# Kernel tuning notes

Measured on AMD Instinct MI355X. Metric: run time of the kernel, lower is better.

Reference implementation:

```python
import jax, jax.numpy as jnp
import numpy as np

# NSA hyperparams (match init_kwargs)
KS, ST, SEL, TOPN, WIN = 32, 16, 64, 16, 512
NEG = -1e30  # additive mask value (finite so fp32 softmax stays stable)


def setup_inputs() -> dict:
    key = jax.random.key(0)
    ks = jax.random.split(key, 6)
    B, S, Hq, Hk, D, Dv = 1, 2048, 16, 2, 128, 128
    q = jax.random.normal(ks[0], (B, S, Hq, D), jnp.float32)
    k = jax.random.normal(ks[1], (B, S, Hk, D), jnp.float32)
    v = jax.random.normal(ks[2], (B, S, Hk, Dv), jnp.float32)
    # learned per-position compression weights for K and V blocks
    w_cmp_k = jax.random.normal(ks[3], (KS,), jnp.float32) / KS
    w_cmp_v = jax.random.normal(ks[4], (KS,), jnp.float32) / KS
    # gating head: Linear(qk_head_dim, 3) -> sigmoid
    w_gate = jax.random.normal(ks[5], (D, 3), jnp.float32) * 0.02
    b_gate = jnp.zeros((3,), jnp.float32)
    return dict(q=q, k=k, v=v, w_cmp_k=w_cmp_k, w_cmp_v=w_cmp_v,
                w_gate=w_gate, b_gate=b_gate)


def _nsa(q, k, v, w_cmp_k, w_cmp_v, w_gate, b_gate):
    B, S, Hq, D = q.shape
    Hk = k.shape[2]
    G = Hq // Hk                      # GQA group size
    Dv = v.shape[-1]
    scale = D ** -0.5
    t_pos = jnp.arange(S)

    # ---- 1. compressed-KV attention (CompressAttn) ----
    T = (S - KS) // ST + 1            # number of compressed blocks
    widx = jnp.arange(T)[:, None] * ST + jnp.arange(KS)[None, :]   # [T, KS]
    cmp_k = jnp.einsum('btknd,k->btnd', k[:, widx], w_cmp_k)        # [B,T,Hk,D]
    cmp_v = jnp.einsum('btknd,k->btnd', v[:, widx], w_cmp_v)        # [B,T,Hk,Dv]

    qg = q.reshape(B, S, Hk, G, D)
    s_cmp = jnp.einsum('bsngd,btnd->bngst', qg, cmp_k) * scale      # [B,Hk,G,S,T]
    blk_end = jnp.arange(T) * ST + KS - 1
    cmp_mask = blk_end[None, :] <= t_pos[:, None]                   # [S,T] block fully past
    p_cmp = jax.nn.softmax(jnp.where(cmp_mask, s_cmp, NEG), axis=-1)
    p_cmp = p_cmp * cmp_mask          # zero rows with no visible block
    cmp_o = jnp.einsum('bngst,btnd->bsngd', p_cmp, cmp_v).reshape(B, S, Hq, Dv)

    # ---- 2. top-n selection-block scoring (select_for_fwd_bwd) ----
    NSel = S // SEL
    starts = jnp.arange(T) * ST
    b_lo = starts // SEL
    b_hi = (starts + KS - 1) // SEL
    bidx = jnp.arange(NSel)
    # map compressed-block probs onto overlapping selection blocks
    Mmap = ((bidx[None, :] >= b_lo[:, None]) & (bidx[None, :] <= b_hi[:, None])).astype(q.dtype)  # [T,NSel]
    p_slc = jnp.einsum('bngst,tm->bnsm', p_cmp, Mmap)               # sum over group g -> [B,Hk,S,NSel]

    cur_blk = t_pos // SEL
    blk_causal = (bidx[None, :] * SEL) <= t_pos[:, None]            # [S,NSel]
    forced = (bidx[None, :] == 0) | (bidx[None, :] == cur_blk[:, None])
    blk_score = jnp.where(forced, -NEG, p_slc)                      # always keep block 0 + current
    blk_score = jnp.where(blk_causal, blk_score, NEG)
    vals, inds = jax.lax.top_k(blk_score, TOPN)                     # [B,Hk,S,TOPN]
    valid = (vals > NEG / 2).astype(q.dtype)
    sel_blk_mask = (jax.nn.one_hot(inds, NSel, dtype=q.dtype) * valid[..., None]).sum(-2) > 0  # [B,Hk,S,NSel]

    # ---- 3. block-sparse selected attention (select_attn) ----
    tok_sel_mask = jnp.repeat(sel_blk_mask, SEL, axis=-1)           # [B,Hk,S,S]
    causal = t_pos[None, :] <= t_pos[:, None]                       # [S,S]
    tok_sel_mask = tok_sel_mask & causal
    s_tok = jnp.einsum('bsngd,bjnd->bngsj', qg, k) * scale          # [B,Hk,G,S,S] shared scores
    p_sel = jax.nn.softmax(jnp.where(tok_sel_mask[:, :, None], s_tok, NEG), axis=-1)
    sel_o = jnp.einsum('bngsj,bjnd->bsngd', p_sel, v).reshape(B, S, Hq, Dv)

    win_mask = causal & ((t_pos[:, None] - t_pos[None, :]) <= WIN)
    p_win = jax.nn.softmax(jnp.where(win_mask, s_tok, NEG), axis=-1)
    win_o = jnp.einsum('bngsj,bjnd->bsngd', p_win, v).reshape(B, S, Hq, Dv)

    # ---- 5. learned sigmoid gating combine ----
    gate = jax.nn.sigmoid(jnp.einsum('bshd,dc->bshc', q, w_gate) + b_gate)  # [B,S,Hq,3]
    return (cmp_o * gate[..., 0:1] + sel_o * gate[..., 1:2] + win_o * gate[..., 2:3])


def reference(q, k, v, w_cmp_k, w_cmp_v, w_gate, b_gate):
    return _nsa(q, k, v, w_cmp_k, w_cmp_v, w_gate, b_gate)
```

## Files before the change

### kernel.cpp

```cpp
#include <hip/hip_runtime.h>

#define SS   2048
#define HQ   16
#define HK   2
#define GQ   8
#define DD   128
#define DV   128
#define KS   32
#define ST   16
#define SELB 64
#define TOPN 16
#define WINW 512
#define TT   127
#define NSEL 32
#define QSC  0.12751744f

typedef __attribute__((ext_vector_type(8))) short bf16x8;
typedef __attribute__((ext_vector_type(4))) float f32x4;

#if defined(__has_builtin)
#  if __has_builtin(__builtin_amdgcn_exp2f)
#    define EXP2(x) __builtin_amdgcn_exp2f(x)
#  endif
#endif
#ifndef EXP2
#  define EXP2(x) __expf((x) * 0.6931471805599453f)
#endif

__device__ __forceinline__ short f2bf(float x) {
    union { float f; unsigned u; } a; a.f = x;
    unsigned r = a.u + 0x7FFFu + ((a.u >> 16) & 1u);
    return (short)(r >> 16);
}
__device__ __forceinline__ float bf2f(short b) {
    union { unsigned u; float f; } x; x.u = ((unsigned)(unsigned short)b) << 16; return x.f;
}

__global__ __launch_bounds__(256) void k_prep(
    const float* __restrict__ k, const float* __restrict__ v,
    const float* __restrict__ wck, const float* __restrict__ wcv,
    const float* __restrict__ wg,
    short* __restrict__ kfr, short* __restrict__ vfr,
    short* __restrict__ ckh, short* __restrict__ ckl,
    short* __restrict__ cvfr, short* __restrict__ wgh, short* __restrict__ wgl)
{
    __shared__ float red[256];
    int bid = blockIdx.x, tid = threadIdx.x;
    int lane = tid & 63, quad = (lane >> 4) & 3, l16 = lane & 15;
    if (bid < 256) {
        int tb = bid >> 1, n = bid & 1;
        int kb = tid >> 6;
        int token = tb * 16 + l16;
        int feat = kb * 32 + quad * 8;
        const float* src = &k[(token * HK + n) * DD + feat];
        bf16x8 t;
        #pragma unroll
        for (int e = 0; e < 8; ++e) t[e] = f2bf(src[e]);
        *(bf16x8*)&kfr[(((n * 128 + tb) * 4 + kb) * 64 + lane) * 8] = t;
    } else if (bid < 512) {
        int id = bid - 256;
        int cb = id >> 3, n = (id >> 2) & 1, it = id & 3;
        int frag = it * 4 + (tid >> 6);
        int h = frag >> 3, f = frag & 7;
        int d = f * 16 + l16;
        int tok0 = cb * 64 + h * 32 + quad * 8;
        bf16x8 t;
        #pragma unroll
        for (int e = 0; e < 8; ++e) t[e] = f2bf(v[((tok0 + e) * HK + n) * DV + d]);
        *(bf16x8*)&vfr[((((n * 32 + cb) * 2 + h) * 8 + f) * 64 + lane) * 8] = t;
    } else if (bid < 768) {
        int id = bid - 512;
        int n = id & 1, t = id >> 1;
        int d = tid & 127, jh = tid >> 7;
        float a = 0.f;
        if (t < TT) {
            #pragma unroll
            for (int jj = 0; jj < 16; ++jj) {
                int j = jh * 16 + jj;
                a += k[((t * ST + j) * HK + n) * DD + d] * wck[j];
            }
        }
        red[tid] = a;
        __syncthreads();
        if (tid < 128) {
            float s = red[tid] + red[tid + 128];
            short hi = f2bf(s);
            short lo = f2bf(s - bf2f(hi));
            int tile = t >> 4, l16i = t & 15;
            int kb = d >> 5, qd = (d >> 3) & 3, e = d & 7;
            int off = (((n * 8 + tile) * 4 + kb) * 64 + qd * 16 + l16i) * 8 + e;
            ckh[off] = hi;
            ckl[off] = lo;
        }
    } else if (bid < 1024) {
        int id = bid - 768;
        int n = id & 1, tok = id >> 1;
        int d = tid & 127, jh = tid >> 7;
        float a = 0.f;
        if (tok < TT) {
            #pragma unroll
            for (int jj = 0; jj < 16; ++jj) {
                int j = jh * 16 + jj;
                a += v[((tok * ST + j) * HK + n) * DV + d] * wcv[j];
            }
        }
        red[tid] = a;
        __syncthreads();
        if (tid < 128) {
            float s = red[tid] + red[tid + 128];
            int w2 = d >> 5, half = (d >> 4) & 1, l16i = d & 15;
            int kb = tok >> 5, qd = (tok >> 3) & 3, e = tok & 7;
            cvfr[((((n * 4 + w2) * 2 + half) * 4 + kb) * 64 + qd * 16 + l16i) * 8 + e] = f2bf(s);
        }
    } else {
        int kb = tid >> 6;
        bf16x8 th, tl;
        #pragma unroll
        for (int e = 0; e < 8; ++e) {
            int kidx = kb * 32 + quad * 8 + e;
            float x = (l16 < 3) ? wg[kidx * 3 + l16] : 0.f;
            th[e] = f2bf(x);
            tl[e] = f2bf(x - bf2f(th[e]));
        }
        *(bf16x8*)&wgh[(kb * 64 + lane) * 8] = th;
        *(bf16x8*)&wgl[(kb * 64 + lane) * 8] = tl;
    }
}

__global__ __launch_bounds__(256, 4) void k_fused(
    const float* __restrict__ q,
    const short* __restrict__ ckh, const short* __restrict__ ckl,
    const short* __restrict__ cvfr,
    const short* __restrict__ kfr, const short* __restrict__ vfr,
    const short* __restrict__ wgh, const short* __restrict__ wgl,
    const float* __restrict__ bg,
    float* __restrict__ out)
{
    int r = (int)blockIdx.x & 7, j = (int)blockIdx.x >> 3;
    int sidx = (j < 64) ? (1023 - r * 64 - j) : (r * 64 + (j - 64));
    int s0 = sidx * 2;
    int s1 = s0 + 1;
    int n = blockIdx.y;
    int tid = threadIdx.x;
    int w = tid >> 6, lane = tid & 63, quad = lane >> 4, l16 = lane & 15;

    __shared__ union {
        float p[16][132];
        short Pw[4][16][64];
        float o2[2][16][68];
    } u;
    __shared__ short OselB[16][128];
    __shared__ short cmpO[16][136];
    __shared__ float g3v[16][3];
    __shared__ float pslc2[2][NSEL];
    __shared__ float lw[4][16];
    __shared__ unsigned selMask[2];
    __shared__ unsigned ublk[NSEL];
    __shared__ int shUCnt;

    f32x4 z4 = {0.f, 0.f, 0.f, 0.f};
    const bf16x8 ones8 = {0x3F80, 0x3F80, 0x3F80, 0x3F80, 0x3F80, 0x3F80, 0x3F80, 0x3F80};

    bf16x8 qb[4];
    bf16x8 qlb[4];
    {
        const float* qpg = &q[((s0 + (l16 >> 3)) * HQ + n * GQ + (l16 & 7)) * DD + quad * 8];
        #pragma unroll
        for (int kb = 0; kb < 4; ++kb) {
            f32x4 x = *(const f32x4*)(qpg + kb * 32);
            f32x4 y = *(const f32x4*)(qpg + kb * 32 + 4);
            bf16x8 th, tl;
            #pragma unroll
            for (int j2 = 0; j2 < 4; ++j2) {
                float xs = x[j2] * QSC, ys = y[j2] * QSC;
                th[j2] = f2bf(xs);     tl[j2] = f2bf(xs - bf2f(th[j2]));
                th[4+j2] = f2bf(ys);   tl[4+j2] = f2bf(ys - bf2f(th[4+j2]));
            }
            qb[kb] = th; qlb[kb] = tl;
        }
    }
    if (w == 0) {
        f32x4 gacc = z4;
        #pragma unroll
        for (int kb = 0; kb < 4; ++kb) {
            bf16x8 wh = *(const bf16x8*)&wgh[(kb * 64 + lane) * 8];
            bf16x8 wl = *(const bf16x8*)&wgl[(kb * 64 + lane) * 8];
            gacc = __builtin_amdgcn_mfma_f32_16x16x32_bf16(wh, qb[kb], gacc, 0, 0, 0);
            gacc = __builtin_amdgcn_mfma_f32_16x16x32_bf16(wl, qb[kb], gacc, 0, 0, 0);
            gacc = __builtin_amdgcn_mfma_f32_16x16x32_bf16(wh, qlb[kb], gacc, 0, 0, 0);
        }
        if (quad == 0) {
            #pragma unroll
            for (int r2 = 0; r2 < 3; ++r2) {
                float a = gacc[r2] * (1.f / QSC) + bg[r2];
                g3v[l16][r2] = 1.f / (1.f + __expf(-a));
            }
        }
    }
    for (int tile = w; tile < 8; tile += 4) {
        const short* khp = &ckh[((n * 8 + tile) * 256 + lane) * 8];
        const short* klp = &ckl[((n * 8 + tile) * 256 + lane) * 8];
        f32x4 acc = z4;
        #pragma unroll
        for (int kb = 0; kb < 4; ++kb) {
            bf16x8 ah = *(const bf16x8*)(khp + kb * 512);
            bf16x8 al = *(const bf16x8*)(klp + kb * 512);
            acc = __builtin_amdgcn_mfma_f32_16x16x32_bf16(ah, qb[kb], acc, 0, 0, 0);
            acc = __builtin_amdgcn_mfma_f32_16x16x32_bf16(al, qb[kb], acc, 0, 0, 0);
            acc = __builtin_amdgcn_mfma_f32_16x16x32_bf16(ah, qlb[kb], acc, 0, 0, 0);
        }
        *(f32x4*)&u.p[l16][tile * 16 + quad * 4] = acc;
    }
    __syncthreads();

    int ntt0 = (s0 >= KS - 1) ? min((s0 - (KS - 1)) / ST + 1, TT) : 0;
    int ntt1 = (s1 >= KS - 1) ? min((s1 - (KS - 1)) / ST + 1, TT) : 0;

    #pragma unroll
    for (int rr = 0; rr < 4; ++rr) {
        int row = w * 4 + rr;
        int ntt = (row < 8) ? ntt0 : ntt1;
        int t1 = lane, t2 = lane + 64;
        float v1 = (t1 < ntt) ? u.p[row][t1] : -1e30f;
        float v2 = (t2 < ntt) ? u.p[row][t2] : -1e30f;
        float m = fmaxf(v1, v2);
        #pragma unroll
        for (int o = 32; o > 0; o >>= 1) m = fmaxf(m, __shfl_xor(m, o, 64));
        float e1 = (t1 < ntt) ? EXP2(v1 - m) : 0.f;
        float e2 = (t2 < ntt) ? EXP2(v2 - m) : 0.f;
        float ssum = e1 + e2;
        #pragma unroll
        for (int o = 32; o > 0; o >>= 1) ssum += __shfl_xor(ssum, o, 64);
        float inv = (ntt > 0) ? (1.f / ssum) : 0.f;
        e1 *= inv; e2 *= inv;
        u.p[row][t1] = e1; u.p[row][t2] = e2;
    }
    __syncthreads();

    if (tid < 64) {
        int p01 = tid >> 5, m = tid & 31;
        float a = 0.f;
        for (int dt = -1; dt < 4; ++dt) {
            int t = 4 * m + dt;
            if (t < 0 || t >= TT) continue;
            bool maps = (t / 4 == m) || ((t % 4 == 3) && (t / 4 == m - 1));
            if (!maps) continue;
            for (int g = 0; g < GQ; ++g) a += u.p[p01 * 8 + g][t];
        }
        pslc2[p01][m] = a;
    }
    __syncthreads();

    if (w < 2) {
        int p01 = w;
        int sp = p01 ? s1 : s0;
        int cur = sp / SELB;
        float v;
        if (lane < NSEL) {
            int m = lane;
            if (m == 0 || m == cur) v = 1e30f;
            else if (m * SELB <= sp) v = pslc2[p01][m];
            else v = -1e30f;
        } else v = -1e31f;
        unsigned msk = 0;
        #pragma unroll
        for (int pick = 0; pick < TOPN; ++pick) {
            float bv = v;
            #pragma unroll
            for (int o = 32; o > 0; o >>= 1) bv = fmaxf(bv, __shfl_xor(bv, o, 64));
            unsigned long long b = __ballot(v == bv);
            int best = __ffsll((long long)b) - 1;
            if (bv > -5e29f) msk |= 1u << best;
            if (lane == best) v = -1e31f;
        }
        if (lane == 0) selMask[p01] = msk;
    }
    {
        f32x4 o0 = z4, o1 = z4;
        int d0 = w * 32 + l16;
        const short* cvp = &cvfr[((n * 4 + w) * 512 + lane) * 8];
        const float* prow = &u.p[l16][quad * 8];
        #pragma unroll
        for (int kb = 0; kb < 4; ++kb) {
            f32x4 x = *(const f32x4*)(prow + kb * 32);
            f32x4 y = *(const f32x4*)(prow + kb * 32 + 4);
            bf16x8 pa;
            #pragma unroll
            for (int j2 = 0; j2 < 4; ++j2) { pa[j2] = f2bf(x[j2]); pa[4+j2] = f2bf(y[j2]); }
            bf16x8 vb0 = *(const bf16x8*)(cvp + kb * 512);
            bf16x8 vb1 = *(const bf16x8*)(cvp + 2048 + kb * 512);
            o0 = __builtin_amdgcn_mfma_f32_16x16x32_bf16(pa, vb0, o0, 0, 0, 0);
            o1 = __builtin_amdgcn_mfma_f32_16x16x32_bf16(pa, vb1, o1, 0, 0, 0);
        }
        #pragma unroll
        for (int r2 = 0; r2 < 4; ++r2) {
            int h2 = quad * 4 + r2;
            cmpO[h2][d0]      = f2bf(o0[r2]);
            cmpO[h2][d0 + 16] = f2bf(o1[r2]);
        }
    }
    __syncthreads();

    if (tid == 0) {
        unsigned m0 = selMask[0], m1 = selMask[1], mu = m0 | m1;
        int uc = 0;
        for (int b = 0; b < NSEL; ++b)
            if ((mu >> b) & 1u)
                ublk[uc++] = (unsigned)(b * SELB) | (((m0 >> b) & 1u) << 30) | (((m1 >> b) & 1u) << 31);
        shUCnt = uc;
    }
    __syncthreads();
    int uCnt = shUCnt;
    int j00 = (s0 >= WINW) ? (s0 - WINW) : 0;
    int j01 = (s1 >= WINW) ? (s1 - WINW) : 0;
    int tb0 = j00 & ~63;
    int nBlkB = ((s1 - tb0) >> 6) + 1;

    int sLim = (l16 < 8) ? s0 : s1;
    f32x4 o[8];
    f32x4 lacc;

    char* pwRow = (char*)&u.Pw[w][l16][0];
    int swz = l16 & 7;

    auto run_chunks = [&](int nB, bool selMode) {
        #pragma unroll
        for (int f = 0; f < 8; ++f) o[f] = z4;
        lacc = z4;
        int loWin = selMode ? 0 : ((l16 < 8) ? j00 : j01);
        for (int bi = w; bi < nB; bi += 4) {
            int tstart, vis;
            if (selMode) {
                unsigned e = ublk[bi];
                tstart = (int)(e & 0x0FFFFFFFu);
                vis = (l16 < 8) ? (int)((e >> 30) & 1u) : (int)(e >> 31);
            } else {
                tstart = tb0 + bi * 64;
                vis = 1;
            }
            f32x4 a4[4] = {z4, z4, z4, z4};
            {
                const short* kp = &kfr[((n * 128 + (tstart >> 4)) * 256 + lane) * 8];
                bf16x8 kf[2][4];
                #pragma unroll
                for (int t2 = 0; t2 < 2; ++t2)
                    #pragma unroll
                    for (int kb = 0; kb < 4; ++kb)
                        kf[t2][kb] = *(const bf16x8*)(kp + (t2 * 4 + kb) * 512);
                #pragma unroll
                for (int kb = 0; kb < 4; ++kb) {
                    a4[0] = __builtin_amdgcn_mfma_f32_16x16x32_bf16(kf[0][kb], qb[kb], a4[0], 0, 0, 0);
                    a4[1] = __builtin_amdgcn_mfma_f32_16x16x32_bf16(kf[1][kb], qb[kb], a4[1], 0, 0, 0);
                }
                #pragma unroll
                for (int t2 = 0; t2 < 2; ++t2)
                    #pragma unroll
                    for (int kb = 0; kb < 4; ++kb)
                        kf[t2][kb] = *(const bf16x8*)(kp + ((2 + t2) * 4 + kb) * 512);
                #pragma unroll
                for (int kb = 0; kb < 4; ++kb) {
                    a4[2] = __builtin_amdgcn_mfma_f32_16x16x32_bf16(kf[0][kb], qb[kb], a4[2], 0, 0, 0);
                    a4[3] = __builtin_amdgcn_mfma_f32_16x16x32_bf16(kf[1][kb], qb[kb], a4[3], 0, 0, 0);
                }
            }
            const short* vp = &vfr[((n * 32 + (tstart >> 6)) * 1024 + lane) * 8];
            bf16x8 vf[8];
            #pragma unroll
            for (int f = 0; f < 8; ++f) vf[f] = *(const bf16x8*)(vp + f * 512);
            {
                int lo = loWin - tstart;
                int hi = vis ? (sLim - tstart) : (lo - 1);
                int rngS = hi - lo + 1;
                unsigned rng = (unsigned)(rngS > 0 ? rngS : 0);
                int tb = quad * 4 - lo;
                #pragma unroll
                for (int tile = 0; tile < 4; ++tile) {
                    float ev[4];
                    #pragma unroll
                    for (int r2 = 0; r2 < 4; ++r2) {
                        unsigned uu = (unsigned)(tb + tile * 16 + r2);
                        float ex = EXP2(a4[tile][r2]);
                        ev[r2] = (uu < rng) ? ex : 0.f;
                    }
                    unsigned plo = (__float_as_uint(ev[1]) & 0xFFFF0000u) | (__float_as_uint(ev[0]) >> 16);
                    unsigned phi = (__float_as_uint(ev[3]) & 0xFFFF0000u) | (__float_as_uint(ev[2]) >> 16);
                    uint2 pk; pk.x = plo; pk.y = phi;
                    int chunk = (tile * 2 + (quad >> 1)) ^ swz;
                    *(uint2*)(pwRow + chunk * 16 + (quad & 1) * 8) = pk;
                }
            }
            __builtin_amdgcn_s_waitcnt(0xC07F);
            bf16x8 pa0 = *(const bf16x8*)(pwRow + ((quad ^ swz) * 16));
            bf16x8 pa1 = *(const bf16x8*)(pwRow + (((4 + quad) ^ swz) * 16));
            lacc = __builtin_amdgcn_mfma_f32_16x16x32_bf16(pa0, ones8, lacc, 0, 0, 0);
            lacc = __builtin_amdgcn_mfma_f32_16x16x32_bf16(pa1, ones8, lacc, 0, 0, 0);
            #pragma unroll
            for (int f = 0; f < 8; ++f)
                o[f] = __builtin_amdgcn_mfma_f32_16x16x32_bf16(pa0, vf[f], o[f], 0, 0, 0);
            #pragma unroll
            for (int f = 0; f < 8; ++f)
                o[f] = __builtin_amdgcn_mfma_f32_16x16x32_bf16(pa1, *(const bf16x8*)(vp + (8 + f) * 512), o[f], 0, 0, 0);
        }
    };

    auto combine = [&](bool isA) {
        if (l16 == 0) {
            #pragma unroll
            for (int r2 = 0; r2 < 4; ++r2) lw[w][quad * 4 + r2] = lacc[r2];
        }
        __syncthreads();
        float ltot = lw[0][l16] + lw[1][l16] + lw[2][l16] + lw[3][l16];
        float linv = 1.f / ltot;
        float linvr[4];
        #pragma unroll
        for (int r2 = 0; r2 < 4; ++r2) linvr[r2] = __shfl(linv, quad * 4 + r2, 64);
        #pragma unroll
        for (int half = 0; half < 2; ++half) {
            if (w >= 2) {
                #pragma unroll
                for (int f = 0; f < 4; ++f)
                    #pragma unroll
                    for (int r2 = 0; r2 < 4; ++r2)
                        u.o2[w - 2][quad * 4 + r2][l16 + 16 * f] = o[half * 4 + f][r2];
            }
            __syncthreads();
            if (w < 2) {
                #pragma unroll
                for (int f = 0; f < 4; ++f)
                    #pragma unroll
                    for (int r2 = 0; r2 < 4; ++r2)
                        o[half * 4 + f][r2] += u.o2[w][quad * 4 + r2][l16 + 16 * f];
            }
            __syncthreads();
            if (w == 1) {
                #pragma unroll
                for (int f = 0; f < 4; ++f)
                    #pragma unroll
                    for (int r2 = 0; r2 < 4; ++r2)
                        u.o2[0][quad * 4 + r2][l16 + 16 * f] = o[half * 4 + f][r2];
            }
            __syncthreads();
            if (w == 0) {
                #pragma unroll
                for (int f = 0; f < 4; ++f)
                    #pragma unroll
                    for (int r2 = 0; r2 < 4; ++r2)
                        o[half * 4 + f][r2] += u.o2[0][quad * 4 + r2][l16 + 16 * f];
                if (isA) {
                    #pragma unroll
                    for (int f = 0; f < 4; ++f)
                        #pragma unroll
                        for (int r2 = 0; r2 < 4; ++r2)
                            OselB[quad * 4 + r2][l16 + 16 * (half * 4 + f)] = f2bf(o[half * 4 + f][r2] * linvr[r2]);
                } else {
                    #pragma unroll
                    for (int f = 0; f < 4; ++f)
                        #pragma unroll
                        for (int r2 = 0; r2 < 4; ++r2) {
                            int h2 = quad * 4 + r2;
                            int p = h2 >> 3, g = h2 & 7;
                            int d = l16 + 16 * (half * 4 + f);
                            int ob = ((s0 + p) * HQ + n * GQ + g) * DV + d;
                            float owin = o[half * 4 + f][r2] * linvr[r2];
                            out[ob] = g3v[h2][0] * bf2f(cmpO[h2][d]) + g3v[h2][1] * bf2f(OselB[h2][d]) + g3v[h2][2] * owin;
                        }
                }
            }
            __syncthreads();
        }
    };

    run_chunks(uCnt, true);
    combine(true);
    run_chunks(nBlkB, false);
    combine(false);
}

extern "C" void kernel_launch(void* const* d_in, const int* in_sizes, int n_in,
                              void* d_out, int out_size, void* d_ws, size_t ws_size,
                              hipStream_t stream) {
    const float* q   = (const float*)d_in[0];
    const float* k   = (const float*)d_in[1];
    const float* v   = (const float*)d_in[2];
    const float* wck = (const float*)d_in[3];
    const float* wcv = (const float*)d_in[4];
    const float* wg  = (const float*)d_in[5];
    const float* bg  = (const float*)d_in[6];
    float* out = (float*)d_out;

    short* kfr  = (short*)d_ws;
    short* vfr  = kfr + 2 * 128 * 4 * 64 * 8;
    short* ckh  = vfr + 2 * 32 * 2 * 8 * 64 * 8;
    short* ckl  = ckh + 2 * 8 * 4 * 64 * 8;
    short* cvfr = ckl + 2 * 8 * 4 * 64 * 8;
    short* wgh  = cvfr + 2 * 4 * 2 * 4 * 64 * 8;
    short* wgl  = wgh + 4 * 64 * 8;

    k_prep<<<1025, 256, 0, stream>>>(k, v, wck, wcv, wg, kfr, vfr, ckh, ckl, cvfr, wgh, wgl);
    k_fused<<<dim3(SS / 2, HK), 256, 0, stream>>>(q, ckh, ckl, cvfr, kfr, vfr, wgh, wgl, bg, out);
}
```

Before: 171.2 us.

## Software-pipeline K fragment loads across chunks and simplify block ordering

Restructures the chunk loop so the first half of the next chunk's K fragments is prefetched during the current chunk's softmax and PV work. Loads of the second K half and of V are issued together up front. The launch bound drops from 4 to 3 waves per SIMD to make room for the extra live registers. The block-to-row mapping is also changed from an interleaved heavy/light ordering to a plain descending order, which alters load balance across CUs.

```diff
diff --git a/kernel.cpp b/kernel.cpp
--- a/kernel.cpp
+++ b/kernel.cpp
@@ -127,7 +127,7 @@
     }
 }
 
-__global__ __launch_bounds__(256, 4) void k_fused(
+__global__ __launch_bounds__(256, 3) void k_fused(
     const float* __restrict__ q,
     const short* __restrict__ ckh, const short* __restrict__ ckl,
     const short* __restrict__ cvfr,
@@ -136,9 +136,7 @@
     const float* __restrict__ bg,
     float* __restrict__ out)
 {
-    int r = (int)blockIdx.x & 7, j = (int)blockIdx.x >> 3;
-    int sidx = (j < 64) ? (1023 - r * 64 - j) : (r * 64 + (j - 64));
-    int s0 = sidx * 2;
+    int s0 = (SS - 2) - (int)blockIdx.x * 2;
     int s1 = s0 + 1;
     int n = blockIdx.y;
     int tid = threadIdx.x;
@@ -328,45 +326,54 @@
         for (int f = 0; f < 8; ++f) o[f] = z4;
         lacc = z4;
         int loWin = selMode ? 0 : ((l16 < 8) ? j00 : j01);
-        for (int bi = w; bi < nB; bi += 4) {
-            int tstart, vis;
+        int bi = w;
+        if (bi >= nB) return;
+        auto desc = [&](int b, int& ts, int& vs) {
             if (selMode) {
-                unsigned e = ublk[bi];
-                tstart = (int)(e & 0x0FFFFFFFu);
-                vis = (l16 < 8) ? (int)((e >> 30) & 1u) : (int)(e >> 31);
+                unsigned e = ublk[b];
+                ts = (int)(e & 0x0FFFFFFFu);
+                vs = (l16 < 8) ? (int)((e >> 30) & 1u) : (int)(e >> 31);
             } else {
-                tstart = tb0 + bi * 64;
-                vis = 1;
-            }
+                ts = tb0 + b * 64;
+                vs = 1;
+            }
+        };
+        int tstart, vis;
+        desc(bi, tstart, vis);
+        bf16x8 kfA[8];
+        {
+            const short* kp = &kfr[((n * 128 + (tstart >> 4)) * 256 + lane) * 8];
+            #pragma unroll
+            for (int i2 = 0; i2 < 8; ++i2) kfA[i2] = *(const bf16x8*)(kp + i2 * 512);
+        }
+        while (bi < nB) {
+            const short* kp = &kfr[((n * 128 + (tstart >> 4)) * 256 + lane) * 8];
+            const short* vp = &vfr[((n * 32 + (tstart >> 6)) * 1024 + lane) * 8];
+            bf16x8 kfB[8];
+            #pragma unroll
+            for (int i2 = 0; i2 < 8; ++i2) kfB[i2] = *(const bf16x8*)(kp + (8 + i2) * 512);
+            bf16x8 vf[8];
+            #pragma unroll
+            for (int f = 0; f < 8; ++f) vf[f] = *(const bf16x8*)(vp + f * 512);
             f32x4 a4[4] = {z4, z4, z4, z4};
+            #pragma unroll
+            for (int kb = 0; kb < 4; ++kb) {
+                a4[0] = __builtin_amdgcn_mfma_f32_16x16x32_bf16(kfA[kb],     qb[kb], a4[0], 0, 0, 0);
+                a4[1] = __builtin_amdgcn_mfma_f32_16x16x32_bf16(kfA[4 + kb], qb[kb], a4[1], 0, 0, 0);
+            }
+            #pragma unroll
+            for (int kb = 0; kb < 4; ++kb) {
+                a4[2] = __builtin_amdgcn_mfma_f32_16x16x32_bf16(kfB[kb],     qb[kb], a4[2], 0, 0, 0);
+                a4[3] = __builtin_amdgcn_mfma_f32_16x16x32_bf16(kfB[4 + kb], qb[kb], a4[3], 0, 0, 0);
+            }
+            int nbi = bi + 4;
+            int nts = tstart, nvs = vis;
+            if (nbi < nB) desc(nbi, nts, nvs);
             {
-                const short* kp = &kfr[((n * 128 + (tstart >> 4)) * 256 + lane) * 8];
-                bf16x8 kf[2][4];
+                const short* kpn = &kfr[((n * 128 + (nts >> 4)) * 256 + lane) * 8];
                 #pragma unroll
-                for (int t2 = 0; t2 < 2; ++t2)
-                    #pragma unroll
-                    for (int kb = 0; kb < 4; ++kb)
-                        kf[t2][kb] = *(const bf16x8*)(kp + (t2 * 4 + kb) * 512);
-                #pragma unroll
-                for (int kb = 0; kb < 4; ++kb) {
-                    a4[0] = __builtin_amdgcn_mfma_f32_16x16x32_bf16(kf[0][kb], qb[kb], a4[0], 0, 0, 0);
-                    a4[1] = __builtin_amdgcn_mfma_f32_16x16x32_bf16(kf[1][kb], qb[kb], a4[1], 0, 0, 0);
-                }
-                #pragma unroll
-                for (int t2 = 0; t2 < 2; ++t2)
-                    #pragma unroll
-                    for (int kb = 0; kb < 4; ++kb)
-                        kf[t2][kb] = *(const bf16x8*)(kp + ((2 + t2) * 4 + kb) * 512);
-                #pragma unroll
-                for (int kb = 0; kb < 4; ++kb) {
-                    a4[2] = __builtin_amdgcn_mfma_f32_16x16x32_bf16(kf[0][kb], qb[kb], a4[2], 0, 0, 0);
-                    a4[3] = __builtin_amdgcn_mfma_f32_16x16x32_bf16(kf[1][kb], qb[kb], a4[3], 0, 0, 0);
-                }
-            }
-            const short* vp = &vfr[((n * 32 + (tstart >> 6)) * 1024 + lane) * 8];
-            bf16x8 vf[8];
-            #pragma unroll
-            for (int f = 0; f < 8; ++f) vf[f] = *(const bf16x8*)(vp + f * 512);
+                for (int i2 = 0; i2 < 8; ++i2) kfA[i2] = *(const bf16x8*)(kpn + i2 * 512);
+            }
             {
                 int lo = loWin - tstart;
                 int hi = vis ? (sLim - tstart) : (lo - 1);
@@ -400,6 +407,7 @@
             #pragma unroll
             for (int f = 0; f < 8; ++f)
                 o[f] = __builtin_amdgcn_mfma_f32_16x16x32_bf16(pa1, *(const bf16x8*)(vp + (8 + f) * 512), o[f], 0, 0, 0);
+            bi = nbi; tstart = nts; vis = nvs;
         }
     };
 
```

Measured after the change: 186.4 us. 8.9% more time.
